# Optimization experiments

Hardware: AMD Instinct MI355X
Metric: run time of the kernel (lower is better)

Reference implementation:

```python
import jax, jax.numpy as jnp
import numpy as np

N_NODES = 100000
N_EDGES = 3200000
F_IN = 512
HIDDEN = 16
N_CLASS = 10


def gcn_conv(x, edge_index, W, b):
    """PyG-style GCNConv: sym-normalized aggregation with self-loops.
    out = D^{-1/2} (A + I) D^{-1/2} X W + b
    """
    n = x.shape[0]
    loop = jnp.arange(n, dtype=edge_index.dtype)
    src = jnp.concatenate([edge_index[0], loop])  # [E+N]
    dst = jnp.concatenate([edge_index[1], loop])  # [E+N]
    # degree of target nodes (includes self-loops, so deg >= 1)
    deg = jax.ops.segment_sum(jnp.ones_like(src, dtype=x.dtype), dst, num_segments=n)
    dinv = jax.lax.rsqrt(deg)  # safe: deg >= 1
    norm = dinv[src] * dinv[dst]  # [E+N]
    h = x @ W  # [N, out] — transform before gather (cheaper when out < in)
    msg = h[src] * norm[:, None]  # gather + scale
    out = jax.ops.segment_sum(msg, dst, num_segments=n)  # scatter-add
    return out + b


def setup_inputs() -> dict:
    key = jax.random.key(0)
    k1, k2, k3, k4, k5, k6 = jax.random.split(key, 6)
    x = jax.random.normal(k1, (N_NODES, F_IN), dtype=jnp.float32)
    edge_index = jax.random.randint(k2, (2, N_EDGES), 0, N_NODES, dtype=jnp.int64)
    s1 = 1.0 / np.sqrt(F_IN)
    s2 = 1.0 / np.sqrt(HIDDEN)
    W1 = jax.random.uniform(k3, (F_IN, HIDDEN), jnp.float32, -s1, s1)
    b1 = jax.random.uniform(k4, (HIDDEN,), jnp.float32, -s1, s1)
    W2 = jax.random.uniform(k5, (HIDDEN, N_CLASS), jnp.float32, -s2, s2)
    b2 = jax.random.uniform(k6, (N_CLASS,), jnp.float32, -s2, s2)
    return {"x": x, "edge_index": edge_index, "W1": W1, "b1": b1, "W2": W2, "b2": b2}


def reference(x, edge_index, W1, b1, W2, b2):
    h = gcn_conv(x, edge_index, W1, b1)
    h = jax.nn.relu(h)
    # Dropout(p=0.5) is identity in eval/inference mode
    out = gcn_conv(h, edge_index, W2, b2)
    return out
```

## Files before the change

kernel.cpp:

```cpp
#include <hip/hip_runtime.h>

#define N_NODES 100000
#define N_EDGES 3200000
#define F_IN    512
#define HIDDEN  16
#define N_CLASS 10

#define TILE_R  64
#define KC      64
#define XSTRIDE 68
#define NBLK    ((N_NODES + 255) / 256)

#define NBUCK   196
#define BSH     9
#define EPB     4096
#define NPART   ((N_EDGES + EPB - 1) / EPB)
#define PCAP    18432

__device__ __forceinline__ int load_idx(const void* ei, int is32, long long pos) {
    return is32 ? ((const int*)ei)[pos] : (int)((const long long*)ei)[pos];
}

__global__ void k_zeroi(int* __restrict__ p, int n) {
    int i = blockIdx.x * 256 + threadIdx.x;
    if (i < n) p[i] = 0;
}

__global__ void k_detect(const unsigned* __restrict__ ei, int* __restrict__ det) {
    int t = threadIdx.x;
    unsigned odd = 0;
    for (int i = t; i < 4096; i += 256) odd |= ei[2 * i + 1];
    if (odd) atomicOr(&det[0], 1);
}

__global__ __launch_bounds__(256) void k_bhist(const void* __restrict__ ei,
                                               const int* __restrict__ det,
                                               int* __restrict__ bsize) {
    __shared__ int hist[NBUCK];
    int t = threadIdx.x;
    long long e0 = (long long)blockIdx.x * EPB;
    long long e1 = e0 + EPB; if (e1 > N_EDGES) e1 = N_EDGES;
    int is32 = det[0];
    if (t < NBUCK) hist[t] = 0;
    __syncthreads();
    for (long long e = e0 + t; e < e1; e += 256) {
        int d = load_idx(ei, is32, N_EDGES + e);
        atomicAdd(&hist[d >> BSH], 1);
    }
    __syncthreads();
    if (t < NBUCK && hist[t]) atomicAdd(&bsize[t], hist[t]);
}

__global__ void k_bucketscan(const int* __restrict__ bsize, int* __restrict__ bbase,
                             int* __restrict__ bcur) {
    __shared__ int s[256];
    int t = threadIdx.x;
    int v = (t < NBUCK) ? bsize[t] : 0;
    s[t] = v;
    __syncthreads();
    for (int off = 1; off < 256; off <<= 1) {
        int u = (t >= off) ? s[t - off] : 0;
        __syncthreads();
        s[t] += u;
        __syncthreads();
    }
    if (t < NBUCK) { int ex = s[t] - v; bbase[t] = ex; bcur[t] = ex; }
}

__global__ __launch_bounds__(256) void k_part(const void* __restrict__ ei,
                                              const int* __restrict__ det,
                                              int* __restrict__ bcur,
                                              unsigned* __restrict__ buf) {
    __shared__ int hist[NBUCK];
    __shared__ int base[NBUCK];
    __shared__ int lcur[NBUCK];
    int t = threadIdx.x;
    long long e0 = (long long)blockIdx.x * EPB;
    long long e1 = e0 + EPB; if (e1 > N_EDGES) e1 = N_EDGES;
    int is32 = det[0];
    if (t < NBUCK) { hist[t] = 0; lcur[t] = 0; }
    __syncthreads();
    for (long long e = e0 + t; e < e1; e += 256) {
        int d = load_idx(ei, is32, N_EDGES + e);
        atomicAdd(&hist[d >> BSH], 1);
    }
    __syncthreads();
    if (t < NBUCK) base[t] = hist[t] ? atomicAdd(&bcur[t], hist[t]) : 0;
    __syncthreads();
    for (long long e = e0 + t; e < e1; e += 256) {
        int s = load_idx(ei, is32, e);
        int d = load_idx(ei, is32, (long long)N_EDGES + e);
        int b = d >> BSH;
        int off = atomicAdd(&lcur[b], 1);
        buf[base[b] + off] = ((unsigned)s << BSH) | (unsigned)(d & 511);
    }
}

__global__ __launch_bounds__(256) void k_degb(const unsigned* __restrict__ buf,
                                              const int* __restrict__ bbase,
                                              const int* __restrict__ bsize,
                                              int* __restrict__ deg,
                                              float* __restrict__ dinv) {
    __shared__ int cnt[512];
    int t = threadIdx.x;
    int b = blockIdx.x;
    cnt[t] = 0; cnt[t + 256] = 0;
    __syncthreads();
    int j0 = bbase[b], j1 = j0 + bsize[b];
    for (int j = j0 + t; j < j1; j += 256)
        atomicAdd(&cnt[buf[j] & 511], 1);
    __syncthreads();
    int n = (b << BSH) + t;
    if (n < N_NODES) { deg[n] = cnt[t]; dinv[n] = rsqrtf((float)(cnt[t] + 1)); }
    n += 256;
    if (n < N_NODES) { deg[n] = cnt[t + 256]; dinv[n] = rsqrtf((float)(cnt[t + 256] + 1)); }
}

__global__ void k_bsum(const int* __restrict__ deg, int* __restrict__ bsum) {
    __shared__ int s[256];
    int t = threadIdx.x;
    int i = blockIdx.x * 256 + t;
    s[t] = (i < N_NODES) ? deg[i] : 0;
    __syncthreads();
    for (int off = 128; off > 0; off >>= 1) {
        if (t < off) s[t] += s[t + off];
        __syncthreads();
    }
    if (t == 0) bsum[blockIdx.x] = s[0];
}

__global__ void k_bscan(const int* __restrict__ bsum, int* __restrict__ boff, int nb) {
    __shared__ int s[512];
    int t = threadIdx.x;
    s[t] = (t < nb) ? bsum[t] : 0;
    __syncthreads();
    for (int off = 1; off < 512; off <<= 1) {
        int u = (t >= off) ? s[t - off] : 0;
        __syncthreads();
        s[t] += u;
        __syncthreads();
    }
    if (t < nb) boff[t] = (t == 0) ? 0 : s[t - 1];
}

__global__ void k_rowptr(const int* __restrict__ deg, const int* __restrict__ boff,
                         int* __restrict__ rowptr) {
    __shared__ int s[256];
    int t = threadIdx.x;
    int i = blockIdx.x * 256 + t;
    int v = (i < N_NODES) ? deg[i] : 0;
    s[t] = v;
    __syncthreads();
    for (int off = 1; off < 256; off <<= 1) {
        int u = (t >= off) ? s[t - off] : 0;
        __syncthreads();
        s[t] += u;
        __syncthreads();
    }
    if (i < N_NODES) {
        int ex = s[t] - v + boff[blockIdx.x];
        rowptr[i] = ex;
        if (i == N_NODES - 1) rowptr[N_NODES] = ex + v;
    }
}

__global__ __launch_bounds__(256) void k_place3(const unsigned* __restrict__ buf,
                                                const int* __restrict__ bbase,
                                                const int* __restrict__ bsize,
                                                const int* __restrict__ rowptr,
                                                int* __restrict__ csr) {
    __shared__ int lptr[512];
    __shared__ int outb[PCAP];
    int t = threadIdx.x;
    int b = blockIdx.x;
    int jb = bbase[b];
    int sz = bsize[b];
    int nb0 = b << BSH;
    int csrbase = rowptr[nb0];
    for (int i = t; i < 512; i += 256) {
        int n = nb0 + i;
        lptr[i] = (n < N_NODES) ? rowptr[n] - csrbase : sz;
    }
    __syncthreads();
    for (int j = t; j < sz; j += 256) {
        unsigned p = buf[jb + j];
        int pos = atomicAdd(&lptr[p & 511], 1);
        int s = (int)(p >> BSH);
        if (pos < PCAP) outb[pos] = s;
        else            csr[csrbase + pos] = s;
    }
    __syncthreads();
    int lim = sz < PCAP ? sz : PCAP;
    for (int j = t; j < lim; j += 256) csr[csrbase + j] = outb[j];
}

__global__ void k_wt(const float* __restrict__ W1, float* __restrict__ Wt) {
    int t = blockIdx.x * 256 + threadIdx.x;
    if (t < F_IN * HIDDEN) {
        int k = t >> 9;
        int j = t & (F_IN - 1);
        Wt[t] = W1[j * HIDDEN + k];
    }
}

__global__ __launch_bounds__(256) void k_gemm1(const float* __restrict__ x,
                                               const float* __restrict__ Wt,
                                               const float* __restrict__ dinv,
                                               float* __restrict__ hs) {
    __shared__ float sX[TILE_R * XSTRIDE];
    int t = threadIdx.x;
    int lane = t & 63;
    int rowbase = blockIdx.x * TILE_R;
    int kbase = __builtin_amdgcn_readfirstlane((t >> 6) << 2);
    const float* wk = Wt + kbase * F_IN;

    float4 r[4];
#pragma unroll
    for (int i = 0; i < 4; ++i) {
        int f = i * 256 + t, row = f >> 4, c4 = f & 15;
        int grow = rowbase + row;
        r[i] = make_float4(0.f, 0.f, 0.f, 0.f);
        if (grow < N_NODES)
            r[i] = ((const float4*)(x + (size_t)grow * F_IN))[c4];
    }
    float acc[4] = {};
#pragma unroll 1
    for (int ch = 0; ch < F_IN / KC; ++ch) {
#pragma unroll
        for (int i = 0; i < 4; ++i) {
            int f = i * 256 + t, row = f >> 4, c4 = f & 15;
            *((float4*)&sX[row * XSTRIDE + c4 * 4]) = r[i];
        }
        __syncthreads();
        if (ch + 1 < F_IN / KC) {
#pragma unroll
            for (int i = 0; i < 4; ++i) {
                int f = i * 256 + t, row = f >> 4, c4 = f & 15;
                int grow = rowbase + row;
                r[i] = make_float4(0.f, 0.f, 0.f, 0.f);
                if (grow < N_NODES)
                    r[i] = ((const float4*)(x + (size_t)grow * F_IN + (ch + 1) * KC))[c4];
            }
        }
#pragma unroll
        for (int js = 0; js < KC; js += 4) {
            float4 xv = *((const float4*)&sX[lane * XSTRIDE + js]);
#pragma unroll
            for (int kk = 0; kk < 4; ++kk) {
                const float* wp = wk + kk * F_IN + ch * KC + js;
                acc[kk] += xv.x * wp[0] + xv.y * wp[1] + xv.z * wp[2] + xv.w * wp[3];
            }
        }
        __syncthreads();
    }
    int grow = rowbase + lane;
    if (grow < N_NODES) {
        float di = dinv[grow];
        *((float4*)&hs[(size_t)grow * HIDDEN + kbase]) =
            make_float4(acc[0] * di, acc[1] * di, acc[2] * di, acc[3] * di);
    }
}

__global__ __launch_bounds__(256) void k_agg1(const int* __restrict__ rowptr,
                                              const int* __restrict__ csr,
                                              const float* __restrict__ hs,
                                              const float* __restrict__ dinv,
                                              const float* __restrict__ b1,
                                              const float* __restrict__ W2,
                                              float* __restrict__ ts) {
    __shared__ float sh[16][17];
    int t  = threadIdx.x;
    int ln = t >> 4;
    int k  = t & 15;
    int n  = blockIdx.x * 16 + ln;
    bool valid = n < N_NODES;
    int r0 = valid ? rowptr[n] : 0;
    int r1 = valid ? rowptr[n + 1] : 0;
    float acc = valid ? hs[(size_t)n * HIDDEN + k] : 0.f;
    int j = r0;
    for (; j + 4 <= r1; j += 4) {
        int s0 = csr[j], s1 = csr[j + 1], s2 = csr[j + 2], s3 = csr[j + 3];
        float v0 = hs[(size_t)s0 * HIDDEN + k];
        float v1 = hs[(size_t)s1 * HIDDEN + k];
        float v2 = hs[(size_t)s2 * HIDDEN + k];
        float v3 = hs[(size_t)s3 * HIDDEN + k];
        acc += (v0 + v1) + (v2 + v3);
    }
    for (; j < r1; ++j) acc += hs[(size_t)csr[j] * HIDDEN + k];
    float di = valid ? dinv[n] : 0.f;
    float h = di * acc + b1[k];
    sh[ln][k] = h > 0.f ? h : 0.f;
    __syncthreads();
    int c = (k < N_CLASS) ? k : 0;
    float o = 0.f;
#pragma unroll
    for (int kk = 0; kk < HIDDEN; ++kk) o += sh[ln][kk] * W2[kk * N_CLASS + c];
    if (valid) ts[(size_t)n * 16 + k] = (k < N_CLASS) ? o * di : 0.f;
}

__global__ __launch_bounds__(256) void k_agg2(const int* __restrict__ rowptr,
                                              const int* __restrict__ csr,
                                              const float* __restrict__ ts,
                                              const float* __restrict__ dinv,
                                              const float* __restrict__ b2,
                                              float* __restrict__ out) {
    int t  = threadIdx.x;
    int ln = t >> 4;
    int c  = t & 15;
    int n  = blockIdx.x * 16 + ln;
    if (n >= N_NODES) return;
    int r0 = rowptr[n], r1 = rowptr[n + 1];
    float acc = ts[(size_t)n * 16 + c];
    int j = r0;
    for (; j + 4 <= r1; j += 4) {
        int s0 = csr[j], s1 = csr[j + 1], s2 = csr[j + 2], s3 = csr[j + 3];
        float v0 = ts[(size_t)s0 * 16 + c];
        float v1 = ts[(size_t)s1 * 16 + c];
        float v2 = ts[(size_t)s2 * 16 + c];
        float v3 = ts[(size_t)s3 * 16 + c];
        acc += (v0 + v1) + (v2 + v3);
    }
    for (; j < r1; ++j) acc += ts[(size_t)csr[j] * 16 + c];
    if (c < N_CLASS) out[(size_t)n * N_CLASS + c] = dinv[n] * acc + b2[c];
}

extern "C" void kernel_launch(void* const* d_in, const int* in_sizes, int n_in,
                              void* d_out, int out_size, void* d_ws, size_t ws_size,
                              hipStream_t stream) {
    const float* x  = (const float*)d_in[0];
    const void*  ei = d_in[1];
    const float* W1 = (const float*)d_in[2];
    const float* b1 = (const float*)d_in[3];
    const float* W2 = (const float*)d_in[4];
    const float* b2 = (const float*)d_in[5];
    float* out = (float*)d_out;
    float* ws  = (float*)d_ws;

    float* dinv   = ws;
    int*   deg    = (int*)(ws + 100096);
    int*   rowptr = (int*)(ws + 200192);
    int*   bsum   = (int*)(ws + 300608);
    int*   boff   = (int*)(ws + 301120);
    int*   bsize  = (int*)(ws + 301632);
    int*   bbase  = (int*)(ws + 301888);
    int*   bcur   = (int*)(ws + 302144);
    int*   det    = (int*)(ws + 302400);
    int*   csr    = (int*)(ws + 302464);
    float* hs     = ws + 3502464;
    float* ts     = ws + 5102464;
    float* Wt     = ws + 6702464;
    unsigned* buf = (unsigned*)(ws + 3502464);

    k_zeroi <<<1, 256, 0, stream>>>(bsize, NBUCK);
    k_zeroi <<<1, 64, 0, stream>>>(det, 1);
    k_detect<<<1, 256, 0, stream>>>((const unsigned*)ei, det);

    k_bhist     <<<NPART, 256, 0, stream>>>(ei, det, bsize);
    k_bucketscan<<<1, 256, 0, stream>>>(bsize, bbase, bcur);
    k_part      <<<NPART, 256, 0, stream>>>(ei, det, bcur, buf);
    k_degb      <<<NBUCK, 256, 0, stream>>>(buf, bbase, bsize, deg, dinv);

    k_bsum  <<<NBLK, 256, 0, stream>>>(deg, bsum);
    k_bscan <<<1, 512, 0, stream>>>(bsum, boff, NBLK);
    k_rowptr<<<NBLK, 256, 0, stream>>>(deg, boff, rowptr);
    k_place3<<<NBUCK, 256, 0, stream>>>(buf, bbase, bsize, rowptr, csr);

    k_wt    <<<(F_IN * HIDDEN) / 256, 256, 0, stream>>>(W1, Wt);
    k_gemm1 <<<(N_NODES + TILE_R - 1) / TILE_R, 256, 0, stream>>>(x, Wt, dinv, hs);

    k_agg1  <<<(N_NODES + 15) / 16, 256, 0, stream>>>(rowptr, csr, hs, dinv, b1, W2, ts);
    k_agg2  <<<(N_NODES + 15) / 16, 256, 0, stream>>>(rowptr, csr, ts, dinv, b2, out);
}
```

Measured before the change: 548.8 us.

## Fuse degree count with per-bucket scan and replace tiled GEMM with per-row GEMV

Degree counting, block sums, block scan and rowptr computation are merged into one per-bucket kernel. Each bucket's 512 nodes are contiguous and its edges already start at bbase, so the local exclusive scan plus the bucket base gives rowptr directly. The zero and detect kernels are merged, and the transposed-W kernel is dropped. The shared-memory tiled GEMM is replaced by a one-thread-per-row GEMV that reads the row with float4 loads and reads W1 through wave-uniform loads. The intent is to remove several launches and the extra deg round trip. The risks are the GEMV's uncoalesced row-strided x reads (each thread reads its own 2KB row) and higher register pressure from 16 float4s plus 16 accumulators.

```diff
diff --git a/kernel.cpp b/kernel.cpp
--- a/kernel.cpp
+++ b/kernel.cpp
@@ -6,11 +6,6 @@
 #define HIDDEN  16
 #define N_CLASS 10
 
-#define TILE_R  64
-#define KC      64
-#define XSTRIDE 68
-#define NBLK    ((N_NODES + 255) / 256)
-
 #define NBUCK   196
 #define BSH     9
 #define EPB     4096
@@ -21,13 +16,12 @@
     return is32 ? ((const int*)ei)[pos] : (int)((const long long*)ei)[pos];
 }
 
-__global__ void k_zeroi(int* __restrict__ p, int n) {
-    int i = blockIdx.x * 256 + threadIdx.x;
-    if (i < n) p[i] = 0;
-}
-
-__global__ void k_detect(const unsigned* __restrict__ ei, int* __restrict__ det) {
-    int t = threadIdx.x;
+__global__ void k_init(const unsigned* __restrict__ ei, int* __restrict__ bsize,
+                       int* __restrict__ det) {
+    int t = threadIdx.x;
+    if (t < NBUCK) bsize[t] = 0;
+    if (t == 0) det[0] = 0;
+    __syncthreads();
     unsigned odd = 0;
     for (int i = t; i < 4096; i += 256) odd |= ei[2 * i + 1];
     if (odd) atomicOr(&det[0], 1);
@@ -96,72 +90,34 @@
     }
 }
 
-__global__ __launch_bounds__(256) void k_degb(const unsigned* __restrict__ buf,
-                                              const int* __restrict__ bbase,
-                                              const int* __restrict__ bsize,
-                                              int* __restrict__ deg,
-                                              float* __restrict__ dinv) {
-    __shared__ int cnt[512];
+__global__ __launch_bounds__(256) void k_degscan(const unsigned* __restrict__ buf,
+                                                 const int* __restrict__ bbase,
+                                                 const int* __restrict__ bsize,
+                                                 int* __restrict__ rowptr,
+                                                 float* __restrict__ dinv) {
+    __shared__ int s[512];
     int t = threadIdx.x;
     int b = blockIdx.x;
-    cnt[t] = 0; cnt[t + 256] = 0;
+    s[t] = 0; s[t + 256] = 0;
     __syncthreads();
     int j0 = bbase[b], j1 = j0 + bsize[b];
     for (int j = j0 + t; j < j1; j += 256)
-        atomicAdd(&cnt[buf[j] & 511], 1);
-    __syncthreads();
-    int n = (b << BSH) + t;
-    if (n < N_NODES) { deg[n] = cnt[t]; dinv[n] = rsqrtf((float)(cnt[t] + 1)); }
-    n += 256;
-    if (n < N_NODES) { deg[n] = cnt[t + 256]; dinv[n] = rsqrtf((float)(cnt[t + 256] + 1)); }
-}
-
-__global__ void k_bsum(const int* __restrict__ deg, int* __restrict__ bsum) {
-    __shared__ int s[256];
-    int t = threadIdx.x;
-    int i = blockIdx.x * 256 + t;
-    s[t] = (i < N_NODES) ? deg[i] : 0;
-    __syncthreads();
-    for (int off = 128; off > 0; off >>= 1) {
-        if (t < off) s[t] += s[t + off];
-        __syncthreads();
-    }
-    if (t == 0) bsum[blockIdx.x] = s[0];
-}
-
-__global__ void k_bscan(const int* __restrict__ bsum, int* __restrict__ boff, int nb) {
-    __shared__ int s[512];
-    int t = threadIdx.x;
-    s[t] = (t < nb) ? bsum[t] : 0;
-    __syncthreads();
+        atomicAdd(&s[buf[j] & 511], 1);
+    __syncthreads();
+    int o0 = s[t], o1 = s[t + 256];
     for (int off = 1; off < 512; off <<= 1) {
-        int u = (t >= off) ? s[t - off] : 0;
-        __syncthreads();
-        s[t] += u;
-        __syncthreads();
-    }
-    if (t < nb) boff[t] = (t == 0) ? 0 : s[t - 1];
-}
-
-__global__ void k_rowptr(const int* __restrict__ deg, const int* __restrict__ boff,
-                         int* __restrict__ rowptr) {
-    __shared__ int s[256];
-    int t = threadIdx.x;
-    int i = blockIdx.x * 256 + t;
-    int v = (i < N_NODES) ? deg[i] : 0;
-    s[t] = v;
-    __syncthreads();
-    for (int off = 1; off < 256; off <<= 1) {
-        int u = (t >= off) ? s[t - off] : 0;
-        __syncthreads();
-        s[t] += u;
-        __syncthreads();
-    }
-    if (i < N_NODES) {
-        int ex = s[t] - v + boff[blockIdx.x];
-        rowptr[i] = ex;
-        if (i == N_NODES - 1) rowptr[N_NODES] = ex + v;
-    }
+        int v0 = (t >= off) ? s[t - off] : 0;
+        int v1 = s[t + 256 - off];
+        __syncthreads();
+        s[t] += v0; s[t + 256] += v1;
+        __syncthreads();
+    }
+    int nb0 = b << BSH;
+    int base = bbase[b];
+    int n0 = nb0 + t, n1 = nb0 + t + 256;
+    if (n0 < N_NODES) { rowptr[n0] = base + s[t] - o0;       dinv[n0] = rsqrtf((float)(o0 + 1)); }
+    if (n1 < N_NODES) { rowptr[n1] = base + s[t + 256] - o1; dinv[n1] = rsqrtf((float)(o1 + 1)); }
+    if (b == NBUCK - 1 && t == 0) rowptr[N_NODES] = N_EDGES;
 }
 
 __global__ __launch_bounds__(256) void k_place3(const unsigned* __restrict__ buf,
@@ -194,71 +150,36 @@
     for (int j = t; j < lim; j += 256) csr[csrbase + j] = outb[j];
 }
 
-__global__ void k_wt(const float* __restrict__ W1, float* __restrict__ Wt) {
-    int t = blockIdx.x * 256 + threadIdx.x;
-    if (t < F_IN * HIDDEN) {
-        int k = t >> 9;
-        int j = t & (F_IN - 1);
-        Wt[t] = W1[j * HIDDEN + k];
-    }
-}
-
-__global__ __launch_bounds__(256) void k_gemm1(const float* __restrict__ x,
-                                               const float* __restrict__ Wt,
+__global__ __launch_bounds__(128) void k_gemv1(const float* __restrict__ x,
+                                               const float* __restrict__ W1,
                                                const float* __restrict__ dinv,
                                                float* __restrict__ hs) {
-    __shared__ float sX[TILE_R * XSTRIDE];
-    int t = threadIdx.x;
-    int lane = t & 63;
-    int rowbase = blockIdx.x * TILE_R;
-    int kbase = __builtin_amdgcn_readfirstlane((t >> 6) << 2);
-    const float* wk = Wt + kbase * F_IN;
-
-    float4 r[4];
-#pragma unroll
-    for (int i = 0; i < 4; ++i) {
-        int f = i * 256 + t, row = f >> 4, c4 = f & 15;
-        int grow = rowbase + row;
-        r[i] = make_float4(0.f, 0.f, 0.f, 0.f);
-        if (grow < N_NODES)
-            r[i] = ((const float4*)(x + (size_t)grow * F_IN))[c4];
-    }
-    float acc[4] = {};
+    int n = blockIdx.x * 128 + threadIdx.x;
+    if (n >= N_NODES) return;
+    const float4* xr = (const float4*)(x + (size_t)n * F_IN);
+    float acc[16];
+#pragma unroll
+    for (int k = 0; k < 16; ++k) acc[k] = 0.f;
 #pragma unroll 1
-    for (int ch = 0; ch < F_IN / KC; ++ch) {
-#pragma unroll
-        for (int i = 0; i < 4; ++i) {
-            int f = i * 256 + t, row = f >> 4, c4 = f & 15;
-            *((float4*)&sX[row * XSTRIDE + c4 * 4]) = r[i];
+    for (int ch = 0; ch < F_IN / 64; ++ch) {
+        float4 v[16];
+#pragma unroll
+        for (int i = 0; i < 16; ++i) v[i] = xr[ch * 16 + i];
+#pragma unroll
+        for (int i = 0; i < 16; ++i) {
+            const float* wp = &W1[(ch * 64 + i * 4) * HIDDEN];
+#pragma unroll
+            for (int k = 0; k < 16; ++k)
+                acc[k] += v[i].x * wp[k]      + v[i].y * wp[16 + k]
+                        + v[i].z * wp[32 + k] + v[i].w * wp[48 + k];
         }
-        __syncthreads();
-        if (ch + 1 < F_IN / KC) {
-#pragma unroll
-            for (int i = 0; i < 4; ++i) {
-                int f = i * 256 + t, row = f >> 4, c4 = f & 15;
-                int grow = rowbase + row;
-                r[i] = make_float4(0.f, 0.f, 0.f, 0.f);
-                if (grow < N_NODES)
-                    r[i] = ((const float4*)(x + (size_t)grow * F_IN + (ch + 1) * KC))[c4];
-            }
-        }
-#pragma unroll
-        for (int js = 0; js < KC; js += 4) {
-            float4 xv = *((const float4*)&sX[lane * XSTRIDE + js]);
-#pragma unroll
-            for (int kk = 0; kk < 4; ++kk) {
-                const float* wp = wk + kk * F_IN + ch * KC + js;
-                acc[kk] += xv.x * wp[0] + xv.y * wp[1] + xv.z * wp[2] + xv.w * wp[3];
-            }
-        }
-        __syncthreads();
-    }
-    int grow = rowbase + lane;
-    if (grow < N_NODES) {
-        float di = dinv[grow];
-        *((float4*)&hs[(size_t)grow * HIDDEN + kbase]) =
-            make_float4(acc[0] * di, acc[1] * di, acc[2] * di, acc[3] * di);
-    }
+    }
+    float di = dinv[n];
+    float4* o = (float4*)&hs[(size_t)n * HIDDEN];
+    o[0] = make_float4(acc[0] * di,  acc[1] * di,  acc[2] * di,  acc[3] * di);
+    o[1] = make_float4(acc[4] * di,  acc[5] * di,  acc[6] * di,  acc[7] * di);
+    o[2] = make_float4(acc[8] * di,  acc[9] * di,  acc[10] * di, acc[11] * di);
+    o[3] = make_float4(acc[12] * di, acc[13] * di, acc[14] * di, acc[15] * di);
 }
 
 __global__ __launch_bounds__(256) void k_agg1(const int* __restrict__ rowptr,
@@ -337,37 +258,25 @@
     float* ws  = (float*)d_ws;
 
     float* dinv   = ws;
-    int*   deg    = (int*)(ws + 100096);
-    int*   rowptr = (int*)(ws + 200192);
-    int*   bsum   = (int*)(ws + 300608);
-    int*   boff   = (int*)(ws + 301120);
-    int*   bsize  = (int*)(ws + 301632);
-    int*   bbase  = (int*)(ws + 301888);
-    int*   bcur   = (int*)(ws + 302144);
-    int*   det    = (int*)(ws + 302400);
-    int*   csr    = (int*)(ws + 302464);
-    float* hs     = ws + 3502464;
-    float* ts     = ws + 5102464;
-    float* Wt     = ws + 6702464;
-    unsigned* buf = (unsigned*)(ws + 3502464);
-
-    k_zeroi <<<1, 256, 0, stream>>>(bsize, NBUCK);
-    k_zeroi <<<1, 64, 0, stream>>>(det, 1);
-    k_detect<<<1, 256, 0, stream>>>((const unsigned*)ei, det);
-
+    int*   rowptr = (int*)(ws + 100096);
+    int*   bsize  = (int*)(ws + 200512);
+    int*   bbase  = (int*)(ws + 200768);
+    int*   bcur   = (int*)(ws + 201024);
+    int*   det    = (int*)(ws + 201280);
+    int*   csr    = (int*)(ws + 201344);
+    float* hs     = ws + 3401344;
+    float* ts     = ws + 5001344;
+    unsigned* buf = (unsigned*)(ws + 3401344);
+
+    k_init      <<<1, 256, 0, stream>>>((const unsigned*)ei, bsize, det);
     k_bhist     <<<NPART, 256, 0, stream>>>(ei, det, bsize);
     k_bucketscan<<<1, 256, 0, stream>>>(bsize, bbase, bcur);
     k_part      <<<NPART, 256, 0, stream>>>(ei, det, bcur, buf);
-    k_degb      <<<NBUCK, 256, 0, stream>>>(buf, bbase, bsize, deg, dinv);
-
-    k_bsum  <<<NBLK, 256, 0, stream>>>(deg, bsum);
-    k_bscan <<<1, 512, 0, stream>>>(bsum, boff, NBLK);
-    k_rowptr<<<NBLK, 256, 0, stream>>>(deg, boff, rowptr);
-    k_place3<<<NBUCK, 256, 0, stream>>>(buf, bbase, bsize, rowptr, csr);
-
-    k_wt    <<<(F_IN * HIDDEN) / 256, 256, 0, stream>>>(W1, Wt);
-    k_gemm1 <<<(N_NODES + TILE_R - 1) / TILE_R, 256, 0, stream>>>(x, Wt, dinv, hs);
-
-    k_agg1  <<<(N_NODES + 15) / 16, 256, 0, stream>>>(rowptr, csr, hs, dinv, b1, W2, ts);
-    k_agg2  <<<(N_NODES + 15) / 16, 256, 0, stream>>>(rowptr, csr, ts, dinv, b2, out);
-}
+    k_degscan   <<<NBUCK, 256, 0, stream>>>(buf, bbase, bsize, rowptr, dinv);
+    k_place3    <<<NBUCK, 256, 0, stream>>>(buf, bbase, bsize, rowptr, csr);
+
+    k_gemv1<<<(N_NODES + 127) / 128, 128, 0, stream>>>(x, W1, dinv, hs);
+
+    k_agg1<<<(N_NODES + 15) / 16, 256, 0, stream>>>(rowptr, csr, hs, dinv, b1, W2, ts);
+    k_agg2<<<(N_NODES + 15) / 16, 256, 0, stream>>>(rowptr, csr, ts, dinv, b2, out);
+}
```

Measured after the change: 606.1 us. 10.5% more time.
